# Kernel tuning notes

Measured on AMD Instinct MI355X. Metric: run time of the kernel, lower is better.

## Reference

```python
import jax, jax.numpy as jnp
import numpy as np

NEG_SLOPE = 0.01  # torch nn.LeakyReLU default


def setup_inputs() -> dict:
    key = jax.random.key(0)
    k1, k2 = jax.random.split(key)
    B, L, N = 32, 512, 1024
    X = jax.random.normal(k1, (B, L, N), dtype=jnp.float32)
    W = jax.random.normal(k2, (1, 2 * L), dtype=jnp.float32) * (1.0 / np.sqrt(2 * L))
    return {"X": X, "W": W}


def reference(X, W):
    # X: [B, L, N]; W: [1, 2L] weight of Linear(2L, 1, bias=False)
    L = X.shape[1]
    N = X.shape[2]
    w1 = W[0, :L]   # applied to X[:, :, i]
    w2 = W[0, L:]   # applied to X[:, :, j]
    s1 = jnp.einsum('bln,l->bn', X, w1)  # [B, N]
    s2 = jnp.einsum('bln,l->bn', X, w2)  # [B, N]
    # e[b,i,j] = leaky_relu(s1[b,i] + s2[b,j]) for i != j, 0 on the diagonal
    e = jax.nn.leaky_relu(s1[:, :, None] + s2[:, None, :], NEG_SLOPE)  # [B, N, N]
    diag = jnp.eye(N, dtype=bool)
    e = jnp.where(diag[None, :, :], 0.0, e)
    # softmax over dim=1 (over i), matching torch.softmax(e, dim=1)
    alpha = jax.nn.softmax(e, axis=1)  # [B, N, N]
    # h = bmm(alpha, X^T)^T: h[b,l,i] = sum_j alpha[b,i,j] * X[b,l,j]
    h = jnp.einsum('bij,blj->bli', alpha, X)  # [B, L, N]
    return jax.nn.sigmoid(h)
```

## Files before the change

### kernel.cpp

```cpp
#include <hip/hip_runtime.h>
#include <hip/hip_bf16.h>

#define BATCH 32
#define LSEQ  512
#define NDIM  1024
#define NSPLIT 16

typedef __attribute__((ext_vector_type(8))) short bf16x8;
typedef __attribute__((ext_vector_type(4))) float f32x4;

__device__ __forceinline__ unsigned short f2bf(float x) {
    __hip_bfloat16 h = __float2bfloat16(x);
    return __builtin_bit_cast(unsigned short, h);
}

__global__ __launch_bounds__(256) void prep_kernel(
    const float* __restrict__ X, const float* __restrict__ W,
    unsigned short* __restrict__ Xb, float* __restrict__ P1, float* __restrict__ P2)
{
    __shared__ float sw[2 * LSEQ];
    int tid = threadIdx.x;
    for (int i = tid; i < 2 * LSEQ; i += 256) sw[i] = W[i];
    __syncthreads();

    int b  = blockIdx.y;
    int sp = blockIdx.x;
    int l0 = sp * (LSEQ / NSPLIT);
    size_t base = ((size_t)b * LSEQ + l0) * NDIM + tid * 4;
    const float* xp = X + base;
    unsigned short* xbp = Xb + base;

    float a0=0,a1=0,a2=0,a3=0, c0=0,c1=0,c2=0,c3=0;
    for (int l = 0; l < LSEQ / NSPLIT; ++l) {
        float4 x = *(const float4*)(xp + (size_t)l * NDIM);
        float w1 = sw[l0 + l], w2 = sw[LSEQ + l0 + l];
        a0 = fmaf(x.x, w1, a0); a1 = fmaf(x.y, w1, a1);
        a2 = fmaf(x.z, w1, a2); a3 = fmaf(x.w, w1, a3);
        c0 = fmaf(x.x, w2, c0); c1 = fmaf(x.y, w2, c1);
        c2 = fmaf(x.z, w2, c2); c3 = fmaf(x.w, w2, c3);
        ushort4 u; u.x = f2bf(x.x); u.y = f2bf(x.y); u.z = f2bf(x.z); u.w = f2bf(x.w);
        *(ushort4*)(xbp + (size_t)l * NDIM) = u;
    }
    size_t po = ((size_t)sp * BATCH + b) * NDIM + tid * 4;
    *(float4*)(P1 + po) = make_float4(a0, a1, a2, a3);
    *(float4*)(P2 + po) = make_float4(c0, c1, c2, c3);
}

__global__ __launch_bounds__(256) void reduce_kernel(
    const float* __restrict__ P1, const float* __restrict__ P2,
    float* __restrict__ s1, float* __restrict__ s2)
{
    int o = blockIdx.x * 256 + threadIdx.x;
    float a = 0.f, c = 0.f;
    #pragma unroll
    for (int sp = 0; sp < NSPLIT; ++sp) {
        a += P1[(size_t)sp * BATCH * NDIM + o];
        c += P2[(size_t)sp * BATCH * NDIM + o];
    }
    s1[o] = a; s2[o] = c;
}

__global__ __launch_bounds__(256) void rowstats_kernel(
    const float* __restrict__ s1, const float* __restrict__ s2,
    float* __restrict__ m, float* __restrict__ rd)
{
    int wid = threadIdx.x >> 6, lane = threadIdx.x & 63;
    int r = blockIdx.x * 4 + wid;
    int b = r >> 10, j = r & 1023;
    const float* s1b = s1 + b * NDIM;
    float s2j = s2[r];

    float e[16];
    float mx = -1e30f;
    #pragma unroll
    for (int t = 0; t < 16; ++t) {
        int i = lane + 64 * t;
        float v = s1b[i] + s2j;
        v = v > 0.f ? v : 0.01f * v;
        if (i == j) v = 0.f;
        e[t] = v;
        mx = fmaxf(mx, v);
    }
    #pragma unroll
    for (int off = 32; off; off >>= 1) mx = fmaxf(mx, __shfl_xor(mx, off));
    float sum = 0.f;
    #pragma unroll
    for (int t = 0; t < 16; ++t) sum += __expf(e[t] - mx);
    #pragma unroll
    for (int off = 32; off; off >>= 1) sum += __shfl_xor(sum, off);
    if (lane == 0) { m[r] = mx; rd[r] = 1.0f / sum; }
}

__global__ __launch_bounds__(256) void btgen_kernel(
    const float* __restrict__ s1, const float* __restrict__ s2,
    const float* __restrict__ m, const float* __restrict__ rd,
    unsigned short* __restrict__ Bt)
{
    int wid = threadIdx.x >> 6, lane = threadIdx.x & 63;
    int r = blockIdx.x * 4 + wid;
    int b = r >> 10, i = r & 1023;
    float s1i = s1[r];
    const float* s2b = s2 + b * NDIM;
    const float* mb  = m  + b * NDIM;
    const float* rdb = rd + b * NDIM;
    unsigned short* outp = Bt + (size_t)r * NDIM;

    #pragma unroll
    for (int q = 0; q < 4; ++q) {
        int j0 = q * 256 + lane * 4;
        float4 s2v = *(const float4*)(s2b + j0);
        float4 mv  = *(const float4*)(mb  + j0);
        float4 rv  = *(const float4*)(rdb + j0);
        float ev[4] = { s1i + s2v.x, s1i + s2v.y, s1i + s2v.z, s1i + s2v.w };
        float mm[4] = { mv.x, mv.y, mv.z, mv.w };
        float rr[4] = { rv.x, rv.y, rv.z, rv.w };
        ushort4 u;
        unsigned short us[4];
        #pragma unroll
        for (int k = 0; k < 4; ++k) {
            float e = ev[k];
            e = e > 0.f ? e : 0.01f * e;
            if (j0 + k == i) e = 0.f;
            us[k] = f2bf(__expf(e - mm[k]) * rr[k]);
        }
        u.x = us[0]; u.y = us[1]; u.z = us[2]; u.w = us[3];
        *(ushort4*)(outp + j0) = u;
    }
}

__global__ __launch_bounds__(256) void gemm_kernel(
    const unsigned short* __restrict__ Xb, const unsigned short* __restrict__ Bt,
    float* __restrict__ out)
{
    __shared__ __align__(16) unsigned short Xs[128 * 32];
    __shared__ __align__(16) unsigned short Bs[128 * 32];

    int tid = threadIdx.x, wid = tid >> 6, lane = tid & 63;
    int wm = wid >> 1, wn = wid & 1;

    int flat = blockIdx.x;
    int xcd   = flat & 7;
    int idx   = flat >> 3;
    int bg    = idx >> 5;
    int inner = idx & 31;
    int b  = bg * 8 + xcd;
    int n0 = (inner & 7) * 128;
    int l0 = (inner >> 3) * 128;

    const unsigned short* Xg = Xb + ((size_t)b * LSEQ + l0) * NDIM;
    const unsigned short* Bg = Bt + ((size_t)b * NDIM + n0) * NDIM;

    int rin = lane >> 2, ch = lane & 3;

    f32x4 acc[4][4] = {};

    for (int kb = 0; kb < 32; ++kb) {
        int k0 = kb * 32;
        __syncthreads();
        #pragma unroll
        for (int q = 0; q < 2; ++q) {
            int row = wid * 32 + q * 16 + rin;
            const unsigned short* gx = Xg + (size_t)row * NDIM + k0 + ch * 8;
            const unsigned short* gb = Bg + (size_t)row * NDIM + k0 + ch * 8;
            unsigned short* lx = &Xs[(wid * 32 + q * 16) * 32];
            unsigned short* lb = &Bs[(wid * 32 + q * 16) * 32];
            __builtin_amdgcn_global_load_lds(
                (const __attribute__((address_space(1))) void*)gx,
                (__attribute__((address_space(3))) void*)lx, 16, 0, 0);
            __builtin_amdgcn_global_load_lds(
                (const __attribute__((address_space(1))) void*)gb,
                (__attribute__((address_space(3))) void*)lb, 16, 0, 0);
        }
        __syncthreads();

        bf16x8 av[4], bv[4];
        int rsel = lane & 15, ksel = (lane >> 4) * 8;
        #pragma unroll
        for (int mi = 0; mi < 4; ++mi)
            av[mi] = *(const bf16x8*)&Xs[(wm * 64 + mi * 16 + rsel) * 32 + ksel];
        #pragma unroll
        for (int ni = 0; ni < 4; ++ni)
            bv[ni] = *(const bf16x8*)&Bs[(wn * 64 + ni * 16 + rsel) * 32 + ksel];
        #pragma unroll
        for (int mi = 0; mi < 4; ++mi)
            #pragma unroll
            for (int ni = 0; ni < 4; ++ni)
                acc[mi][ni] = __builtin_amdgcn_mfma_f32_16x16x32_bf16(
                    av[mi], bv[ni], acc[mi][ni], 0, 0, 0);
    }

    float* outb = out + ((size_t)b * LSEQ + l0) * NDIM + n0;
    int rq = lane >> 4, cl = lane & 15;
    #pragma unroll
    for (int mi = 0; mi < 4; ++mi)
        #pragma unroll
        for (int ni = 0; ni < 4; ++ni) {
            int col = wn * 64 + ni * 16 + cl;
            #pragma unroll
            for (int r2 = 0; r2 < 4; ++r2) {
                int row = wm * 64 + mi * 16 + rq * 4 + r2;
                float v = acc[mi][ni][r2];
                outb[(size_t)row * NDIM + col] = 1.0f / (1.0f + __expf(-v));
            }
        }
}

extern "C" void kernel_launch(void* const* d_in, const int* in_sizes, int n_in,
                              void* d_out, int out_size, void* d_ws, size_t ws_size,
                              hipStream_t stream) {
    (void)in_sizes; (void)n_in; (void)out_size; (void)ws_size;
    const float* X = (const float*)d_in[0];
    const float* W = (const float*)d_in[1];
    float* out = (float*)d_out;

    float* s1 = (float*)d_ws;
    float* s2 = s1 + BATCH * NDIM;
    float* mrow = s2 + BATCH * NDIM;
    float* rd = mrow + BATCH * NDIM;
    float* P1 = rd + BATCH * NDIM;
    float* P2 = P1 + (size_t)NSPLIT * BATCH * NDIM;
    unsigned short* Xb = (unsigned short*)(P2 + (size_t)NSPLIT * BATCH * NDIM);
    unsigned short* Bt = Xb + (size_t)BATCH * LSEQ * NDIM;

    prep_kernel<<<dim3(NSPLIT, BATCH), 256, 0, stream>>>(X, W, Xb, P1, P2);
    reduce_kernel<<<(BATCH * NDIM) / 256, 256, 0, stream>>>(P1, P2, s1, s2);
    rowstats_kernel<<<(BATCH * NDIM) / 4, 256, 0, stream>>>(s1, s2, mrow, rd);
    btgen_kernel<<<(BATCH * NDIM) / 4, 256, 0, stream>>>(s1, s2, mrow, rd, Bt);
    gemm_kernel<<<1024, 256, 0, stream>>>(Xb, Bt, out);
}
```

Measured before the change: 204.2 us.

## Generate softmax attention tile on the fly inside GEMM, merge stats kernels

Removes the materialized bf16 attention matrix by computing exp(leaky(s1+s2))*rd directly into LDS inside the GEMM k-loop. The reduction of partial scores and the column softmax denominators are fused into one stats kernel, and the max subtraction is dropped. This eliminates a large global write/read of the NxN matrix per batch and two launches. In exchange it adds exp work in the GEMM loop and loses overflow protection for large scores.

```diff
diff --git a/kernel.cpp b/kernel.cpp
--- a/kernel.cpp
+++ b/kernel.cpp
@@ -46,91 +46,56 @@
     *(float4*)(P2 + po) = make_float4(c0, c1, c2, c3);
 }
 
-__global__ __launch_bounds__(256) void reduce_kernel(
+__global__ __launch_bounds__(256) void stats_kernel(
     const float* __restrict__ P1, const float* __restrict__ P2,
-    float* __restrict__ s1, float* __restrict__ s2)
+    float* __restrict__ s1, float* __restrict__ s2, float* __restrict__ rd)
 {
-    int o = blockIdx.x * 256 + threadIdx.x;
-    float a = 0.f, c = 0.f;
-    #pragma unroll
-    for (int sp = 0; sp < NSPLIT; ++sp) {
-        a += P1[(size_t)sp * BATCH * NDIM + o];
-        c += P2[(size_t)sp * BATCH * NDIM + o];
-    }
-    s1[o] = a; s2[o] = c;
-}
-
-__global__ __launch_bounds__(256) void rowstats_kernel(
-    const float* __restrict__ s1, const float* __restrict__ s2,
-    float* __restrict__ m, float* __restrict__ rd)
-{
-    int wid = threadIdx.x >> 6, lane = threadIdx.x & 63;
-    int r = blockIdx.x * 4 + wid;
-    int b = r >> 10, j = r & 1023;
-    const float* s1b = s1 + b * NDIM;
-    float s2j = s2[r];
-
-    float e[16];
-    float mx = -1e30f;
-    #pragma unroll
-    for (int t = 0; t < 16; ++t) {
-        int i = lane + 64 * t;
-        float v = s1b[i] + s2j;
-        v = v > 0.f ? v : 0.01f * v;
-        if (i == j) v = 0.f;
-        e[t] = v;
-        mx = fmaxf(mx, v);
-    }
-    #pragma unroll
-    for (int off = 32; off; off >>= 1) mx = fmaxf(mx, __shfl_xor(mx, off));
-    float sum = 0.f;
-    #pragma unroll
-    for (int t = 0; t < 16; ++t) sum += __expf(e[t] - mx);
-    #pragma unroll
-    for (int off = 32; off; off >>= 1) sum += __shfl_xor(sum, off);
-    if (lane == 0) { m[r] = mx; rd[r] = 1.0f / sum; }
-}
-
-__global__ __launch_bounds__(256) void btgen_kernel(
-    const float* __restrict__ s1, const float* __restrict__ s2,
-    const float* __restrict__ m, const float* __restrict__ rd,
-    unsigned short* __restrict__ Bt)
-{
-    int wid = threadIdx.x >> 6, lane = threadIdx.x & 63;
-    int r = blockIdx.x * 4 + wid;
-    int b = r >> 10, i = r & 1023;
-    float s1i = s1[r];
-    const float* s2b = s2 + b * NDIM;
-    const float* mb  = m  + b * NDIM;
-    const float* rdb = rd + b * NDIM;
-    unsigned short* outp = Bt + (size_t)r * NDIM;
+    __shared__ float s1s[NDIM];
+    __shared__ float s2s[128];
+    int t = threadIdx.x;
+    int b = blockIdx.x >> 3, sl = blockIdx.x & 7;
+    int j0 = sl * 128;
 
     #pragma unroll
     for (int q = 0; q < 4; ++q) {
-        int j0 = q * 256 + lane * 4;
-        float4 s2v = *(const float4*)(s2b + j0);
-        float4 mv  = *(const float4*)(mb  + j0);
-        float4 rv  = *(const float4*)(rdb + j0);
-        float ev[4] = { s1i + s2v.x, s1i + s2v.y, s1i + s2v.z, s1i + s2v.w };
-        float mm[4] = { mv.x, mv.y, mv.z, mv.w };
-        float rr[4] = { rv.x, rv.y, rv.z, rv.w };
-        ushort4 u;
-        unsigned short us[4];
-        #pragma unroll
-        for (int k = 0; k < 4; ++k) {
-            float e = ev[k];
-            e = e > 0.f ? e : 0.01f * e;
-            if (j0 + k == i) e = 0.f;
-            us[k] = f2bf(__expf(e - mm[k]) * rr[k]);
-        }
-        u.x = us[0]; u.y = us[1]; u.z = us[2]; u.w = us[3];
-        *(ushort4*)(outp + j0) = u;
-    }
+        int n = q * 256 + t;
+        float a = 0.f;
+        #pragma unroll
+        for (int sp = 0; sp < NSPLIT; ++sp)
+            a += P1[((size_t)sp * BATCH + b) * NDIM + n];
+        s1s[n] = a;
+        if (sl == 0) s1[b * NDIM + n] = a;
+    }
+    if (t < 128) {
+        int j = j0 + t;
+        float c = 0.f;
+        #pragma unroll
+        for (int sp = 0; sp < NSPLIT; ++sp)
+            c += P2[((size_t)sp * BATCH + b) * NDIM + j];
+        s2s[t] = c;
+        s2[b * NDIM + j] = c;
+    }
+    __syncthreads();
+
+    int jl = t >> 1, half = t & 1;
+    int jg = j0 + jl;
+    float s2j = s2s[jl];
+    float sum = 0.f;
+    int i0 = half * 512;
+    for (int i = i0; i < i0 + 512; ++i) {
+        float v = s1s[i] + s2j;
+        v = fmaxf(v, 0.01f * v);
+        if (i == jg) v = 0.f;
+        sum += __expf(v);
+    }
+    sum += __shfl_xor(sum, 1);
+    if (half == 0) rd[b * NDIM + jg] = 1.0f / sum;
 }
 
 __global__ __launch_bounds__(256) void gemm_kernel(
-    const unsigned short* __restrict__ Xb, const unsigned short* __restrict__ Bt,
-    float* __restrict__ out)
+    const unsigned short* __restrict__ Xb,
+    const float* __restrict__ s1, const float* __restrict__ s2,
+    const float* __restrict__ rd, float* __restrict__ out)
 {
     __shared__ __align__(16) unsigned short Xs[128 * 32];
     __shared__ __align__(16) unsigned short Bs[128 * 32];
@@ -148,28 +113,53 @@
     int l0 = (inner >> 3) * 128;
 
     const unsigned short* Xg = Xb + ((size_t)b * LSEQ + l0) * NDIM;
-    const unsigned short* Bg = Bt + ((size_t)b * NDIM + n0) * NDIM;
+    const float* s2b = s2 + b * NDIM;
+    const float* rdb = rd + b * NDIM;
 
     int rin = lane >> 2, ch = lane & 3;
+
+    int an   = tid >> 1;
+    int koff = (tid & 1) * 16;
+    float s1i = s1[b * NDIM + n0 + an];
 
     f32x4 acc[4][4] = {};
 
     for (int kb = 0; kb < 32; ++kb) {
         int k0 = kb * 32;
         __syncthreads();
+
         #pragma unroll
         for (int q = 0; q < 2; ++q) {
             int row = wid * 32 + q * 16 + rin;
             const unsigned short* gx = Xg + (size_t)row * NDIM + k0 + ch * 8;
-            const unsigned short* gb = Bg + (size_t)row * NDIM + k0 + ch * 8;
             unsigned short* lx = &Xs[(wid * 32 + q * 16) * 32];
-            unsigned short* lb = &Bs[(wid * 32 + q * 16) * 32];
             __builtin_amdgcn_global_load_lds(
                 (const __attribute__((address_space(1))) void*)gx,
                 (__attribute__((address_space(3))) void*)lx, 16, 0, 0);
-            __builtin_amdgcn_global_load_lds(
-                (const __attribute__((address_space(1))) void*)gb,
-                (__attribute__((address_space(3))) void*)lb, 16, 0, 0);
+        }
+
+        {
+            int kg0 = k0 + koff;
+            float sv[16], rv[16];
+            #pragma unroll
+            for (int q = 0; q < 4; ++q) {
+                float4 s4 = *(const float4*)(s2b + kg0 + q * 4);
+                float4 r4 = *(const float4*)(rdb + kg0 + q * 4);
+                sv[q*4+0]=s4.x; sv[q*4+1]=s4.y; sv[q*4+2]=s4.z; sv[q*4+3]=s4.w;
+                rv[q*4+0]=r4.x; rv[q*4+1]=r4.y; rv[q*4+2]=r4.z; rv[q*4+3]=r4.w;
+            }
+            bf16x8 v0, v1;
+            #pragma unroll
+            for (int k = 0; k < 16; ++k) {
+                float v = s1i + sv[k];
+                v = fmaxf(v, 0.01f * v);
+                if (n0 + an == kg0 + k) v = 0.f;
+                float a = __expf(v) * rv[k];
+                unsigned short u = f2bf(a);
+                if (k < 8) v0[k] = (short)u; else v1[k - 8] = (short)u;
+            }
+            *(bf16x8*)&Bs[an * 32 + koff]     = v0;
+            *(bf16x8*)&Bs[an * 32 + koff + 8] = v1;
         }
         __syncthreads();
 
@@ -215,16 +205,12 @@
 
     float* s1 = (float*)d_ws;
     float* s2 = s1 + BATCH * NDIM;
-    float* mrow = s2 + BATCH * NDIM;
-    float* rd = mrow + BATCH * NDIM;
+    float* rd = s2 + BATCH * NDIM;
     float* P1 = rd + BATCH * NDIM;
     float* P2 = P1 + (size_t)NSPLIT * BATCH * NDIM;
     unsigned short* Xb = (unsigned short*)(P2 + (size_t)NSPLIT * BATCH * NDIM);
-    unsigned short* Bt = Xb + (size_t)BATCH * LSEQ * NDIM;
 
     prep_kernel<<<dim3(NSPLIT, BATCH), 256, 0, stream>>>(X, W, Xb, P1, P2);
-    reduce_kernel<<<(BATCH * NDIM) / 256, 256, 0, stream>>>(P1, P2, s1, s2);
-    rowstats_kernel<<<(BATCH * NDIM) / 4, 256, 0, stream>>>(s1, s2, mrow, rd);
-    btgen_kernel<<<(BATCH * NDIM) / 4, 256, 0, stream>>>(s1, s2, mrow, rd, Bt);
-    gemm_kernel<<<1024, 256, 0, stream>>>(Xb, Bt, out);
-}
+    stats_kernel<<<256, 256, 0, stream>>>(P1, P2, s1, s2, rd);
+    gemm_kernel<<<1024, 256, 0, stream>>>(Xb, s1, s2, rd, out);
+}
```

New measurement: 212.4 us. +4.0%, slower.
